# Performance work log

Hardware: AMD Instinct MI355X
Metric: run time of the kernel (lower is better)

Reference implementation:

```python
import jax, jax.numpy as jnp
import numpy as np
import math

# Dimensions (see shape_source)
B, C, NH = 4, 256, 8
VP, VW = 6, 16   # vertical: patches-per-window (outer), windows (inner)
HP, HW = 32, 3   # horizontal: patches-per-window (outer), windows (inner)
NW, P = VW * HW, VP * HP   # 48 windows, 192 patches per window
GRID = 96                   # patch grid is 96x96
SHIFT = (HP // 2, VP // 2)  # (16, 3) = (window_shape[0]//2, window_shape[1]//2)
FF = 4 * C
SCALE = 1.0 / math.sqrt(C)  # source divides by sqrt(embedding_dim), not head_dim


def setup_inputs() -> dict:
    key = jax.random.key(0)
    ks = jax.random.split(key, 17)
    std = 0.02
    n = lambda k, s: (jax.random.normal(k, s, dtype=jnp.float32) * std)
    return {
        "embeddings": jax.random.normal(ks[0], (B, GRID, GRID, C), dtype=jnp.float32),
        "ln1_g": jnp.ones((C,), jnp.float32), "ln1_b": jnp.zeros((C,), jnp.float32),
        "wq": n(ks[1], (C, C)), "bq": jnp.zeros((C,), jnp.float32),
        "wk": n(ks[2], (C, C)), "bk": jnp.zeros((C,), jnp.float32),
        "wv": n(ks[3], (C, C)), "bv": jnp.zeros((C,), jnp.float32),
        "pos_bias": n(ks[4], (NH, P, P)),
        "ln2_g": jnp.ones((C,), jnp.float32), "ln2_b": jnp.zeros((C,), jnp.float32),
        "w1": n(ks[5], (C, FF)), "b1": jnp.zeros((FF,), jnp.float32),
        "w2": n(ks[6], (FF, C)), "b2": jnp.zeros((C,), jnp.float32),
    }


def _ln(x, g, b, eps=1e-5):
    m = jnp.mean(x, axis=-1, keepdims=True)
    v = jnp.mean(jnp.square(x - m), axis=-1, keepdims=True)
    return (x - m) * jax.lax.rsqrt(v + eps) * g + b


def reference(embeddings, ln1_g, ln1_b, wq, bq, wk, bk, wv, bv, pos_bias,
              ln2_g, ln2_b, w1, b1, w2, b2):
    x = jnp.roll(embeddings, SHIFT, axis=(1, 2))
    # part: H=(VP outer, VW inner), W=(HP outer, HW inner) -> [B, NW, P, C]
    p = x.reshape(B, VP, VW, HP, HW, C).transpose(0, 2, 4, 1, 3, 5).reshape(B, NW, P, C)
    y = _ln(p, ln1_g, ln1_b)
    def heads(w, b):
        return (y @ w + b).reshape(B, NW, P, NH, C // NH).transpose(0, 1, 3, 2, 4)
    q, k, v = heads(wq, bq), heads(wk, bk), heads(wv, bv)  # [B, NW, NH, P, Dh]
    logits = jnp.einsum('bwhpd,bwhqd->bwhpq', q, k) * SCALE + pos_bias
    attn = jax.nn.softmax(logits, axis=-1)
    sa = jnp.einsum('bwhpq,bwhqd->bwhpd', attn, v)
    sa = sa.transpose(0, 1, 3, 2, 4).reshape(B, NW, P, C)
    a = p + sa
    h = _ln(a, ln2_g, ln2_b)
    ff = jax.nn.gelu(h @ w1 + b1, approximate=False) @ w2 + b2
    out = a + ff
    # join: inverse of part
    o = out.reshape(B, VW, HW, VP, HP, C).transpose(0, 3, 1, 4, 2, 5).reshape(B, GRID, GRID, C)
    return jnp.roll(o, (-SHIFT[0], -SHIFT[1]), axis=(1, 2))
```

## Files before the change

kernel.cpp:

```cpp
#include <hip/hip_runtime.h>
#include <hip/hip_bf16.h>
#include <cstdint>

using bf16x8 = __attribute__((ext_vector_type(8))) short;
using f32x4  = __attribute__((ext_vector_type(4))) float;
using bf16_t = __hip_bfloat16;

#define DEVI static __device__ __forceinline__

constexpr int kB = 4, kC = 256, kNH = 8, kDh = 32;
constexpr int kVP = 6, kVW = 16, kHP = 32, kHW = 3;
constexpr int kNW = 48, kP = 192, kGRID = 96;
constexpr int kRows = kB * kNW * kP;
constexpr int kFF = 1024;
constexpr float kScale = 0.0625f;

DEVI void row_coords(int row, int& b, int& g1, int& g2) {
  int b_  = row / (kNW * kP);
  int rem = row - b_ * (kNW * kP);
  int w = rem / kP;
  int p = rem - w * kP;
  int vw = w / kHW, hw = w - vw * kHW;
  int vp = p >> 5,  hp = p & 31;
  int r  = vp * kVW + vw;
  int cc = hp * kHW + hw;
  g1 = r + 80;  if (g1 >= kGRID) g1 -= kGRID;
  g2 = cc + 93; if (g2 >= kGRID) g2 -= kGRID;
  b = b_;
}

DEVI float bf2f(short s) {
  union { unsigned u; float f; } c;
  c.u = ((unsigned)(unsigned short)s) << 16;
  return c.f;
}
DEVI short f2bf(float f) {
  bf16_t h = __float2bfloat16(f);
  return *reinterpret_cast<short*>(&h);
}

DEVI void gload16(const void* g, void* l) {
  __builtin_amdgcn_global_load_lds(
      (__attribute__((address_space(1))) void*)(uintptr_t)g,
      (__attribute__((address_space(3))) void*)(uintptr_t)l, 16, 0, 0);
}

DEVI float gelu_fast(float v) {
  const float t = v * 0.7978845608f * (1.f + 0.044715f * v * v);
  const float e = __expf(fminf(-2.f * t, 60.f));
  return 0.5f * v * (1.f + (1.f - e) / (1.f + e));
}

__global__ __launch_bounds__(256) void k_wconv(
    const float* __restrict__ wq, const float* __restrict__ wk,
    const float* __restrict__ wv, const float* __restrict__ w1,
    const float* __restrict__ w2, bf16_t* __restrict__ W) {
  const int i = blockIdx.x * 256 + threadIdx.x;
  if (i < 196608) {
    const int n = i >> 8, k = i & 255;
    const float* src = n < 256 ? wq : (n < 512 ? wk : wv);
    W[i] = __float2bfloat16(src[k * 256 + (n & 255)]);
  } else if (i < 458752) {
    const int j = i - 196608;
    const int n = j >> 8, k = j & 255;
    W[i] = __float2bfloat16(w1[k * 1024 + n]);
  } else if (i < 720896) {
    const int j = i - 458752;
    const int n = j >> 10, k = j & 1023;
    W[i] = __float2bfloat16(w2[k * 256 + n]);
  }
}

__global__ __launch_bounds__(256) void k_ln1(const float* __restrict__ emb,
    const float* __restrict__ gam, const float* __restrict__ bet,
    bf16_t* __restrict__ Y) {
  const int wave = threadIdx.x >> 6, lane = threadIdx.x & 63;
  #pragma unroll
  for (int rr = 0; rr < 2; ++rr) {
    const int row = blockIdx.x * 8 + wave * 2 + rr;
    int b, g1, g2; row_coords(row, b, g1, g2);
    const float* src = emb + (((size_t)b * kGRID + g1) * kGRID + g2) * kC;
    float4 x = *reinterpret_cast<const float4*>(src + lane * 4);
    float s  = x.x + x.y + x.z + x.w;
    float sq = x.x*x.x + x.y*x.y + x.z*x.z + x.w*x.w;
    #pragma unroll
    for (int off = 32; off; off >>= 1) { s += __shfl_xor(s, off); sq += __shfl_xor(sq, off); }
    const float mean = s * (1.f / kC);
    const float rstd = rsqrtf(sq * (1.f / kC) - mean * mean + 1e-5f);
    const float4 g4 = *reinterpret_cast<const float4*>(gam + lane * 4);
    const float4 b4 = *reinterpret_cast<const float4*>(bet + lane * 4);
    short4 o;
    o.x = f2bf((x.x - mean) * rstd * g4.x + b4.x);
    o.y = f2bf((x.y - mean) * rstd * g4.y + b4.y);
    o.z = f2bf((x.z - mean) * rstd * g4.z + b4.z);
    o.w = f2bf((x.w - mean) * rstd * g4.w + b4.w);
    *reinterpret_cast<short4*>(Y + (size_t)row * kC + lane * 4) = o;
  }
}

__global__ __launch_bounds__(256) void k_ln2(const float* __restrict__ emb,
    const bf16_t* __restrict__ SA,
    const float* __restrict__ gam, const float* __restrict__ bet,
    float* __restrict__ A, bf16_t* __restrict__ H) {
  const int wave = threadIdx.x >> 6, lane = threadIdx.x & 63;
  #pragma unroll
  for (int rr = 0; rr < 2; ++rr) {
    const int row = blockIdx.x * 8 + wave * 2 + rr;
    int b, g1, g2; row_coords(row, b, g1, g2);
    const float* src = emb + (((size_t)b * kGRID + g1) * kGRID + g2) * kC;
    float4 x = *reinterpret_cast<const float4*>(src + lane * 4);
    short4 sv = *reinterpret_cast<const short4*>(SA + (size_t)row * kC + lane * 4);
    x.x += bf2f(sv.x); x.y += bf2f(sv.y); x.z += bf2f(sv.z); x.w += bf2f(sv.w);
    *reinterpret_cast<float4*>(A + (size_t)row * kC + lane * 4) = x;
    float s  = x.x + x.y + x.z + x.w;
    float sq = x.x*x.x + x.y*x.y + x.z*x.z + x.w*x.w;
    #pragma unroll
    for (int off = 32; off; off >>= 1) { s += __shfl_xor(s, off); sq += __shfl_xor(sq, off); }
    const float mean = s * (1.f / kC);
    const float rstd = rsqrtf(sq * (1.f / kC) - mean * mean + 1e-5f);
    const float4 g4 = *reinterpret_cast<const float4*>(gam + lane * 4);
    const float4 b4 = *reinterpret_cast<const float4*>(bet + lane * 4);
    short4 o;
    o.x = f2bf((x.x - mean) * rstd * g4.x + b4.x);
    o.y = f2bf((x.y - mean) * rstd * g4.y + b4.y);
    o.z = f2bf((x.z - mean) * rstd * g4.z + b4.z);
    o.w = f2bf((x.w - mean) * rstd * g4.w + b4.w);
    *reinterpret_cast<short4*>(H + (size_t)row * kC + lane * 4) = o;
  }
}

template <int KDIM, int EPI, int GX>
__global__ __launch_bounds__(256, 4) void k_gemm3(
    const bf16_t* __restrict__ Amat, const bf16_t* __restrict__ BT,
    const float* __restrict__ bias0, const float* __restrict__ bias1,
    const float* __restrict__ bias2,
    bf16_t* __restrict__ Obf, const float* __restrict__ Ares,
    float* __restrict__ Out) {
  __shared__ short sm[16384];
  bf16_t* const As0 = (bf16_t*)&sm[0];
  bf16_t* const As1 = (bf16_t*)&sm[4096];
  bf16_t* const Bs0 = (bf16_t*)&sm[8192];
  bf16_t* const Bs1 = (bf16_t*)&sm[12288];
  const int tid = threadIdx.x;
  const int wave = tid >> 6, lane = tid & 63;
  const int lr = lane & 15, kg4 = lane >> 4;
  const int nwg = (kRows / 128) * GX;
  const int wg = (blockIdx.x & 7) * (nwg >> 3) + (blockIdx.x >> 3);
  const int m0 = (wg / GX) * 128, n0 = (wg % GX) * 128;
  const int wm = (wave >> 1) * 64, wn = (wave & 1) * 64;
  const int srow = lane >> 2;
  const int scol = ((lane & 3) ^ (srow & 3)) << 3;

  auto stage = [&](bf16_t* aDst, bf16_t* bDst, int k0) {
    #pragma unroll
    for (int i = 0; i < 2; ++i) {
      const int c = wave * 2 + i;
      const int row = c * 16 + srow;
      gload16(Amat + (size_t)(m0 + row) * KDIM + k0 + scol, aDst + c * 512);
      gload16(BT   + (size_t)(n0 + row) * KDIM + k0 + scol, bDst + c * 512);
    }
  };

  f32x4 acc[4][4] = {};
  auto compute = [&](const bf16_t* aSrc, const bf16_t* bSrc) {
    bf16x8 af[4], bq[4];
    #pragma unroll
    for (int m = 0; m < 4; ++m) {
      const int r = wm + m * 16 + lr;
      af[m] = *reinterpret_cast<const bf16x8*>(aSrc + r * 32 + ((kg4 ^ (r & 3)) << 3));
    }
    #pragma unroll
    for (int n = 0; n < 4; ++n) {
      const int r = wn + n * 16 + lr;
      bq[n] = *reinterpret_cast<const bf16x8*>(bSrc + r * 32 + ((kg4 ^ (r & 3)) << 3));
    }
    #pragma unroll
    for (int m = 0; m < 4; ++m)
      #pragma unroll
      for (int n = 0; n < 4; ++n)
        acc[m][n] = __builtin_amdgcn_mfma_f32_16x16x32_bf16(af[m], bq[n], acc[m][n], 0, 0, 0);
  };

  stage(As0, Bs0, 0);
  __syncthreads();
  constexpr int NT = KDIM / 32;
  #pragma unroll
  for (int t = 0; t < NT; ++t) {
    if (t + 1 < NT) stage(((t + 1) & 1) ? As1 : As0, ((t + 1) & 1) ? Bs1 : Bs0,
                          (t + 1) * 32);
    compute((t & 1) ? As1 : As0, (t & 1) ? Bs1 : Bs0);
    __syncthreads();
  }

  if constexpr (EPI == 0 || EPI == 1) {
    short* scr = &sm[wave * 4096];
    const int colbase = n0 + wn;
    const float* bp;
    int cb;
    if constexpr (EPI == 0) {
      const int which = colbase >> 8;
      bp = which == 0 ? bias0 : (which == 1 ? bias1 : bias2);
      cb = colbase & 255;
    } else { bp = bias0; cb = colbase; }
    #pragma unroll
    for (int m = 0; m < 4; ++m)
      #pragma unroll
      for (int n = 0; n < 4; ++n)
        #pragma unroll
        for (int r = 0; r < 4; ++r) {
          const int lrow = m * 16 + kg4 * 4 + r;
          const int lcol = n * 16 + lr;
          float v = acc[m][n][r] + bp[cb + lcol];
          if constexpr (EPI == 1) v = gelu_fast(v);
          scr[lrow * 64 + lcol] = f2bf(v);
        }
    const int rl = lane >> 3, cl = (lane & 7) * 8;
    bf16_t* const obase = (EPI == 0)
        ? Obf + (size_t)(colbase >> 8) * kRows * kC
        : Obf;
    const int ld = (EPI == 0) ? kC : kFF;
    #pragma unroll
    for (int p = 0; p < 8; ++p) {
      const int lrow = p * 8 + rl;
      bf16x8 v = *reinterpret_cast<const bf16x8*>(&scr[lrow * 64 + cl]);
      *reinterpret_cast<bf16x8*>(
          obase + (size_t)(m0 + wm + lrow) * ld + cb + cl) = v;
    }
  } else {
    float* scrf = reinterpret_cast<float*>(&sm[wave * 4096]);
    #pragma unroll
    for (int h = 0; h < 2; ++h) {
      #pragma unroll
      for (int m = 0; m < 4; ++m)
        #pragma unroll
        for (int nn = 0; nn < 2; ++nn) {
          const int n = h * 2 + nn;
          #pragma unroll
          for (int r = 0; r < 4; ++r)
            scrf[(m * 16 + kg4 * 4 + r) * 32 + nn * 16 + lr] =
                acc[m][n][r] + bias0[n0 + wn + n * 16 + lr];
        }
      const int rl = lane >> 3, cl = (lane & 7) * 4;
      #pragma unroll
      for (int p = 0; p < 8; ++p) {
        const int lrow = p * 8 + rl;
        const int row = m0 + wm + lrow;
        const int col = n0 + wn + h * 32 + cl;
        float4 v = *reinterpret_cast<const float4*>(&scrf[lrow * 32 + cl]);
        const float4 a4 = *reinterpret_cast<const float4*>(
            &Ares[(size_t)row * kC + col]);
        v.x += a4.x; v.y += a4.y; v.z += a4.z; v.w += a4.w;
        int b, g1, g2; row_coords(row, b, g1, g2);
        *reinterpret_cast<float4*>(
            &Out[(((size_t)b * kGRID + g1) * kGRID + g2) * kC + col]) = v;
      }
    }
  }
}

constexpr int kKsPad = 40;
constexpr int kVtPad = 200;
constexpr int kPlPad = 200;
__global__ __launch_bounds__(256) void k_attn(
    const bf16_t* __restrict__ Q, const bf16_t* __restrict__ K,
    const bf16_t* __restrict__ V, const float* __restrict__ pos,
    bf16_t* __restrict__ SA) {
  __shared__ short Ks[kP * kKsPad];
  __shared__ short Vt[kDh * kVtPad];
  __shared__ short Pl[4 * 16 * kPlPad];
  const int bw = blockIdx.x >> 3, h = blockIdx.x & 7;
  const int rowbase = bw * kP, colbase = h * kDh;
  const int tid = threadIdx.x, wave = tid >> 6, lane = tid & 63;
  const int lr = lane & 15, kg = lane >> 4;
  const int wq0 = wave * 48;
  const float* pb = pos + (size_t)h * kP * kP;

  #pragma unroll
  for (int i = 0; i < 3; ++i) {
    const int c = tid + i * 256;
    const int row = c >> 2, dch = (c & 3) * 8;
    const size_t gbase = (size_t)(rowbase + row) * kC + colbase + dch;
    bf16x8 kv = *reinterpret_cast<const bf16x8*>(K + gbase);
    *reinterpret_cast<bf16x8*>(&Ks[row * kKsPad + dch]) = kv;
    bf16x8 vv = *reinterpret_cast<const bf16x8*>(V + gbase);
    #pragma unroll
    for (int e = 0; e < 8; ++e) Vt[(dch + e) * kVtPad + row] = vv[e];
  }
  __syncthreads();

  for (int m = 0; m < 3; ++m) {
    const int rbase = wq0 + m * 16;
    bf16x8 aq = *reinterpret_cast<const bf16x8*>(
        Q + (size_t)(rowbase + rbase + lr) * kC + colbase + kg * 8);
    f32x4 s[12];
    #pragma unroll
    for (int n = 0; n < 12; ++n) {
      bf16x8 bk = *reinterpret_cast<const bf16x8*>(&Ks[(n * 16 + lr) * kKsPad + kg * 8]);
      s[n] = __builtin_amdgcn_mfma_f32_16x16x32_bf16(aq, bk, (f32x4){0.f, 0.f, 0.f, 0.f}, 0, 0, 0);
    }
    float mx[4] = {-1e30f, -1e30f, -1e30f, -1e30f};
    #pragma unroll
    for (int n = 0; n < 12; ++n) {
      #pragma unroll
      for (int r = 0; r < 4; ++r) {
        const float lg = fmaf(s[n][r], kScale,
                              pb[(size_t)(rbase + kg * 4 + r) * kP + n * 16 + lr]);
        s[n][r] = lg;
        mx[r] = fmaxf(mx[r], lg);
      }
    }
    #pragma unroll
    for (int r = 0; r < 4; ++r)
      #pragma unroll
      for (int off = 8; off; off >>= 1) mx[r] = fmaxf(mx[r], __shfl_xor(mx[r], off));
    float sm4[4] = {0.f, 0.f, 0.f, 0.f};
    #pragma unroll
    for (int n = 0; n < 12; ++n)
      #pragma unroll
      for (int r = 0; r < 4; ++r) {
        const float e = __expf(s[n][r] - mx[r]);
        s[n][r] = e;
        sm4[r] += e;
      }
    #pragma unroll
    for (int r = 0; r < 4; ++r) {
      #pragma unroll
      for (int off = 8; off; off >>= 1) sm4[r] += __shfl_xor(sm4[r], off);
      sm4[r] = 1.f / sm4[r];
    }
    #pragma unroll
    for (int n = 0; n < 12; ++n)
      #pragma unroll
      for (int r = 0; r < 4; ++r)
        Pl[(wave * 16 + kg * 4 + r) * kPlPad + n * 16 + lr] = f2bf(s[n][r] * sm4[r]);
    f32x4 o0 = {0.f, 0.f, 0.f, 0.f}, o1 = {0.f, 0.f, 0.f, 0.f};
    #pragma unroll
    for (int kk = 0; kk < 6; ++kk) {
      bf16x8 ap = *reinterpret_cast<const bf16x8*>(&Pl[(wave * 16 + lr) * kPlPad + kk * 32 + kg * 8]);
      bf16x8 b0 = *reinterpret_cast<const bf16x8*>(&Vt[lr * kVtPad + kk * 32 + kg * 8]);
      bf16x8 b1 = *reinterpret_cast<const bf16x8*>(&Vt[(16 + lr) * kVtPad + kk * 32 + kg * 8]);
      o0 = __builtin_amdgcn_mfma_f32_16x16x32_bf16(ap, b0, o0, 0, 0, 0);
      o1 = __builtin_amdgcn_mfma_f32_16x16x32_bf16(ap, b1, o1, 0, 0, 0);
    }
    short* scr2 = &Pl[wave * 16 * kPlPad];
    #pragma unroll
    for (int r = 0; r < 4; ++r) {
      scr2[(kg * 4 + r) * 32 + lr]      = f2bf(o0[r]);
      scr2[(kg * 4 + r) * 32 + 16 + lr] = f2bf(o1[r]);
    }
    {
      const int rrow = lane >> 2, c0 = (lane & 3) * 8;
      bf16x8 v = *reinterpret_cast<const bf16x8*>(&scr2[rrow * 32 + c0]);
      *reinterpret_cast<bf16x8*>(
          SA + (size_t)(rowbase + rbase + rrow) * kC + colbase + c0) = v;
    }
  }
}

extern "C" void kernel_launch(void* const* d_in, const int* in_sizes, int n_in,
                              void* d_out, int out_size, void* d_ws, size_t ws_size,
                              hipStream_t stream) {
  const float* emb  = (const float*)d_in[0];
  const float* ln1g = (const float*)d_in[1];
  const float* ln1b = (const float*)d_in[2];
  const float* wq   = (const float*)d_in[3];
  const float* bq   = (const float*)d_in[4];
  const float* wk   = (const float*)d_in[5];
  const float* bk   = (const float*)d_in[6];
  const float* wv   = (const float*)d_in[7];
  const float* bv   = (const float*)d_in[8];
  const float* pos  = (const float*)d_in[9];
  const float* ln2g = (const float*)d_in[10];
  const float* ln2b = (const float*)d_in[11];
  const float* w1   = (const float*)d_in[12];
  const float* b1   = (const float*)d_in[13];
  const float* w2   = (const float*)d_in[14];
  const float* b2   = (const float*)d_in[15];

  char* ws = (char*)d_ws;
  const size_t nYb = (size_t)kRows * kC * 2;
  bf16_t* Y    = (bf16_t*)(ws);
  bf16_t* Qb   = (bf16_t*)(ws + nYb);
  bf16_t* SAb  = (bf16_t*)(ws + nYb * 4);
  float*  Abuf = (float*) (ws + nYb * 5);
  bf16_t* H    = (bf16_t*)(ws + nYb * 5 + (size_t)kRows * kC * 4);
  bf16_t* G    = (bf16_t*)(ws);
  bf16_t* W    = (bf16_t*)(ws + nYb * 5 + (size_t)kRows * kC * 4 + nYb);
  bf16_t* WqkvT = W;
  bf16_t* W1T   = W + 768 * 256;
  bf16_t* W2T   = W1T + 1024 * 256;

  k_wconv<<<2816, 256, 0, stream>>>(wq, wk, wv, w1, w2, W);
  k_ln1<<<kRows / 8, 256, 0, stream>>>(emb, ln1g, ln1b, Y);
  k_gemm3<256, 0, 6><<<(kRows / 128) * 6, 256, 0, stream>>>(
      Y, WqkvT, bq, bk, bv, Qb, nullptr, nullptr);
  k_attn<<<kB * kNW * kNH, 256, 0, stream>>>(
      Qb, Qb + (size_t)kRows * kC, Qb + 2 * (size_t)kRows * kC, pos, SAb);
  k_ln2<<<kRows / 8, 256, 0, stream>>>(emb, SAb, ln2g, ln2b, Abuf, H);
  k_gemm3<256, 1, 8><<<(kRows / 128) * 8, 256, 0, stream>>>(
      H, W1T, b1, nullptr, nullptr, G, nullptr, nullptr);
  k_gemm3<1024, 2, 2><<<(kRows / 128) * 2, 256, 0, stream>>>(
      G, W2T, b2, nullptr, nullptr, nullptr, Abuf, (float*)d_out);
}
```

Baseline: 184.1 us.

## Hand-schedule GEMM main loop with explicit waitcnts, raw barriers and swizzled epilogue

The GEMM kernel's LDS fragment reads become inline ds_read_b128, and __syncthreads is replaced by explicit vmcnt/lgkmcnt waits plus s_barrier and sched_barrier fences. MFMA issue priority is also raised with s_setprio. The goal is to let the next tile's global-to-LDS loads overlap the current tile's MFMAs without a full drain at each barrier. The epilogue scratch buffers gain an XOR swizzle to cut LDS bank conflicts, and the GELU tanh form is rewritten as an equivalent sigmoid that needs fewer ops. The risk is the hand-tuned vmcnt counts and barrier placement, which could cause races if wrong.

```diff
diff --git a/kernel.cpp b/kernel.cpp
--- a/kernel.cpp
+++ b/kernel.cpp
@@ -45,10 +45,15 @@
       (__attribute__((address_space(3))) void*)(uintptr_t)l, 16, 0, 0);
 }
 
+DEVI bf16x8 ds_read_b128(uint32_t byte_off) {
+  bf16x8 v;
+  asm volatile("ds_read_b128 %0, %1" : "=v"(v) : "v"(byte_off));
+  return v;
+}
+
 DEVI float gelu_fast(float v) {
-  const float t = v * 0.7978845608f * (1.f + 0.044715f * v * v);
-  const float e = __expf(fminf(-2.f * t, 60.f));
-  return 0.5f * v * (1.f + (1.f - e) / (1.f + e));
+  const float t2 = v * 1.5957691216f * (1.f + 0.044715f * v * v);
+  return v / (1.f + __expf(fminf(-t2, 60.f)));
 }
 
 __global__ __launch_bounds__(256) void k_wconv(
@@ -130,7 +135,7 @@
 }
 
 template <int KDIM, int EPI, int GX>
-__global__ __launch_bounds__(256, 4) void k_gemm3(
+__global__ __launch_bounds__(256, 4) void k_gemm6(
     const bf16_t* __restrict__ Amat, const bf16_t* __restrict__ BT,
     const float* __restrict__ bias0, const float* __restrict__ bias1,
     const float* __restrict__ bias2,
@@ -161,36 +166,51 @@
     }
   };
 
+  const uint32_t aOff0 = (uint32_t)(uintptr_t)As0;
+  const uint32_t aOff1 = (uint32_t)(uintptr_t)As1;
+  const uint32_t bOff0 = (uint32_t)(uintptr_t)Bs0;
+  const uint32_t bOff1 = (uint32_t)(uintptr_t)Bs1;
+
   f32x4 acc[4][4] = {};
-  auto compute = [&](const bf16_t* aSrc, const bf16_t* bSrc) {
+  auto compute = [&](uint32_t aBase, uint32_t bBase) {
     bf16x8 af[4], bq[4];
     #pragma unroll
     for (int m = 0; m < 4; ++m) {
       const int r = wm + m * 16 + lr;
-      af[m] = *reinterpret_cast<const bf16x8*>(aSrc + r * 32 + ((kg4 ^ (r & 3)) << 3));
+      af[m] = ds_read_b128(aBase + r * 64 + ((kg4 ^ (r & 3)) << 4));
     }
     #pragma unroll
     for (int n = 0; n < 4; ++n) {
       const int r = wn + n * 16 + lr;
-      bq[n] = *reinterpret_cast<const bf16x8*>(bSrc + r * 32 + ((kg4 ^ (r & 3)) << 3));
-    }
+      bq[n] = ds_read_b128(bBase + r * 64 + ((kg4 ^ (r & 3)) << 4));
+    }
+    asm volatile("s_waitcnt lgkmcnt(0)" ::: "memory");
+    __builtin_amdgcn_sched_barrier(0);
+    __builtin_amdgcn_s_setprio(1);
     #pragma unroll
     for (int m = 0; m < 4; ++m)
       #pragma unroll
       for (int n = 0; n < 4; ++n)
         acc[m][n] = __builtin_amdgcn_mfma_f32_16x16x32_bf16(af[m], bq[n], acc[m][n], 0, 0, 0);
+    __builtin_amdgcn_s_setprio(0);
   };
 
   stage(As0, Bs0, 0);
-  __syncthreads();
   constexpr int NT = KDIM / 32;
   #pragma unroll
   for (int t = 0; t < NT; ++t) {
-    if (t + 1 < NT) stage(((t + 1) & 1) ? As1 : As0, ((t + 1) & 1) ? Bs1 : Bs0,
-                          (t + 1) * 32);
-    compute((t & 1) ? As1 : As0, (t & 1) ? Bs1 : Bs0);
-    __syncthreads();
-  }
+    if (t + 1 < NT) {
+      stage(((t + 1) & 1) ? As1 : As0, ((t + 1) & 1) ? Bs1 : Bs0, (t + 1) * 32);
+      asm volatile("s_waitcnt vmcnt(4)" ::: "memory");
+    } else {
+      asm volatile("s_waitcnt vmcnt(0)" ::: "memory");
+    }
+    __builtin_amdgcn_sched_barrier(0);
+    __builtin_amdgcn_s_barrier();
+    compute((t & 1) ? aOff1 : aOff0, (t & 1) ? bOff1 : bOff0);
+    __builtin_amdgcn_s_barrier();
+  }
+  __builtin_amdgcn_sched_barrier(0);
 
   if constexpr (EPI == 0 || EPI == 1) {
     short* scr = &sm[wave * 4096];
@@ -212,7 +232,8 @@
           const int lcol = n * 16 + lr;
           float v = acc[m][n][r] + bp[cb + lcol];
           if constexpr (EPI == 1) v = gelu_fast(v);
-          scr[lrow * 64 + lcol] = f2bf(v);
+          const int sc = lcol ^ ((lrow & 3) << 4);
+          scr[lrow * 64 + sc] = f2bf(v);
         }
     const int rl = lane >> 3, cl = (lane & 7) * 8;
     bf16_t* const obase = (EPI == 0)
@@ -222,7 +243,8 @@
     #pragma unroll
     for (int p = 0; p < 8; ++p) {
       const int lrow = p * 8 + rl;
-      bf16x8 v = *reinterpret_cast<const bf16x8*>(&scr[lrow * 64 + cl]);
+      const int sc = cl ^ ((lrow & 3) << 4);
+      bf16x8 v = *reinterpret_cast<const bf16x8*>(&scr[lrow * 64 + sc]);
       *reinterpret_cast<bf16x8*>(
           obase + (size_t)(m0 + wm + lrow) * ld + cb + cl) = v;
     }
@@ -236,9 +258,12 @@
         for (int nn = 0; nn < 2; ++nn) {
           const int n = h * 2 + nn;
           #pragma unroll
-          for (int r = 0; r < 4; ++r)
-            scrf[(m * 16 + kg4 * 4 + r) * 32 + nn * 16 + lr] =
+          for (int r = 0; r < 4; ++r) {
+            const int lrow = m * 16 + kg4 * 4 + r;
+            const int lcol = nn * 16 + lr;
+            scrf[lrow * 32 + (lcol ^ ((lrow & 3) << 3))] =
                 acc[m][n][r] + bias0[n0 + wn + n * 16 + lr];
+          }
         }
       const int rl = lane >> 3, cl = (lane & 7) * 4;
       #pragma unroll
@@ -246,7 +271,8 @@
         const int lrow = p * 8 + rl;
         const int row = m0 + wm + lrow;
         const int col = n0 + wn + h * 32 + cl;
-        float4 v = *reinterpret_cast<const float4*>(&scrf[lrow * 32 + cl]);
+        float4 v = *reinterpret_cast<const float4*>(
+            &scrf[lrow * 32 + (cl ^ ((lrow & 3) << 3))]);
         const float4 a4 = *reinterpret_cast<const float4*>(
             &Ares[(size_t)row * kC + col]);
         v.x += a4.x; v.y += a4.y; v.z += a4.z; v.w += a4.w;
@@ -254,6 +280,7 @@
         *reinterpret_cast<float4*>(
             &Out[(((size_t)b * kGRID + g1) * kGRID + g2) * kC + col]) = v;
       }
+      if (h == 0) __builtin_amdgcn_s_barrier();
     }
   }
 }
@@ -392,13 +419,13 @@
 
   k_wconv<<<2816, 256, 0, stream>>>(wq, wk, wv, w1, w2, W);
   k_ln1<<<kRows / 8, 256, 0, stream>>>(emb, ln1g, ln1b, Y);
-  k_gemm3<256, 0, 6><<<(kRows / 128) * 6, 256, 0, stream>>>(
+  k_gemm6<256, 0, 6><<<(kRows / 128) * 6, 256, 0, stream>>>(
       Y, WqkvT, bq, bk, bv, Qb, nullptr, nullptr);
   k_attn<<<kB * kNW * kNH, 256, 0, stream>>>(
       Qb, Qb + (size_t)kRows * kC, Qb + 2 * (size_t)kRows * kC, pos, SAb);
   k_ln2<<<kRows / 8, 256, 0, stream>>>(emb, SAb, ln2g, ln2b, Abuf, H);
-  k_gemm3<256, 1, 8><<<(kRows / 128) * 8, 256, 0, stream>>>(
+  k_gemm6<256, 1, 8><<<(kRows / 128) * 8, 256, 0, stream>>>(
       H, W1T, b1, nullptr, nullptr, G, nullptr, nullptr);
-  k_gemm3<1024, 2, 2><<<(kRows / 128) * 2, 256, 0, stream>>>(
+  k_gemm6<1024, 2, 2><<<(kRows / 128) * 2, 256, 0, stream>>>(
       G, W2T, b2, nullptr, nullptr, nullptr, Abuf, (float*)d_out);
 }
```

Result: faster. 177.3 us (-3.7%).
